# Kernel optimization log

Hardware: AMD Instinct MI355X
Metric: run time of the kernel (lower is better)

The kernel has to match this reference:

```python
import jax, jax.numpy as jnp
import numpy as np

HEADS = 16
SEQ_LEN = 2048
EMB = 1024
BATCH = 2


def setup_inputs() -> dict:
    key = jax.random.key(0)
    ks = jax.random.split(key, 5)
    s = 1.0 / np.sqrt(EMB)
    return {
        "x": jax.random.normal(ks[0], (BATCH, SEQ_LEN, EMB), dtype=jnp.float32),
        "Wk": jax.random.normal(ks[1], (EMB, EMB), dtype=jnp.float32) * s,
        "Wq": jax.random.normal(ks[2], (EMB, EMB), dtype=jnp.float32) * s,
        "Wv": jax.random.normal(ks[3], (EMB, EMB), dtype=jnp.float32) * s,
        "Wu": jax.random.normal(ks[4], (EMB, EMB), dtype=jnp.float32) * s,
        "bu": jnp.zeros((EMB,), dtype=jnp.float32),
    }


def reference(x, Wk, Wq, Wv, Wu, bu):
    B, S, E = x.shape
    H = HEADS
    D = E // H
    # projections (torch Linear: y = x @ W.T); split heads -> [B, H, S, D]
    def proj(W):
        return (x @ W.T).reshape(B, S, H, D).transpose(0, 2, 1, 3)
    q, k, v = proj(Wq), proj(Wk), proj(Wv)
    scores = jnp.einsum("bhsd,bhtd->bhst", q, k) / jnp.sqrt(jnp.float32(D))
    causal_mask = jnp.triu(jnp.ones((S, S), dtype=bool), k=1)  # True above diag
    scores = jnp.where(causal_mask, -jnp.inf, scores)
    attn = jax.nn.softmax(scores, axis=-1)
    ctx = jnp.einsum("bhst,bhtd->bhsd", attn, v)  # [B,H,S,D]
    out = ctx.transpose(0, 2, 1, 3).reshape(B, S, E)
    return out @ Wu.T + bu
```

## Files before the change

### kernel.cpp

```cpp
#include <hip/hip_runtime.h>
#include <hip/hip_bf16.h>

#define HEADS 16
#define SEQ   2048
#define EMB   1024
#define BATCH 2
#define DHEAD 64
#define MTOK  (BATCH * SEQ)

typedef __bf16 bf16x8 __attribute__((ext_vector_type(8)));
typedef float  floatx4 __attribute__((ext_vector_type(4)));

__device__ __forceinline__ void gl_lds16(const void* g, void* l) {
  __builtin_amdgcn_global_load_lds((__attribute__((address_space(1))) void*)(g),
                                   (__attribute__((address_space(3))) void*)(l), 16, 0, 0);
}

__device__ __forceinline__ unsigned short f2bf(float f) {
  __bf16 h = (__bf16)f;
  return __builtin_bit_cast(unsigned short, h);
}

__global__ __launch_bounds__(256) void cvt_kernel(
    const float* __restrict__ x,  const float* __restrict__ wq,
    const float* __restrict__ wk, const float* __restrict__ wv,
    const float* __restrict__ wu,
    unsigned short* __restrict__ xb,  unsigned short* __restrict__ wqb,
    unsigned short* __restrict__ wkb, unsigned short* __restrict__ wvb,
    unsigned short* __restrict__ wub) {
  const int g = blockIdx.x * 256 + threadIdx.x;
  const int XG = (MTOK * EMB) / 4;
  const int WG = (EMB * EMB) / 4;
  const float* src; unsigned short* dst; int off;
  if (g < XG) { src = x; dst = xb; off = g; }
  else {
    int t = g - XG; int wsel = t / WG; off = t - wsel * WG;
    const float* ss[4] = {wq, wk, wv, wu};
    unsigned short* dd[4] = {wqb, wkb, wvb, wub};
    src = ss[wsel]; dst = dd[wsel];
  }
  float4 v = ((const float4*)src)[off];
  ushort4 o;
  o.x = f2bf(v.x); o.y = f2bf(v.y); o.z = f2bf(v.z); o.w = f2bf(v.w);
  ((ushort4*)dst)[off] = o;
}

__global__ __launch_bounds__(256) void gemm_qkv(
    const unsigned short* __restrict__ xb,
    const unsigned short* __restrict__ wqb, const unsigned short* __restrict__ wkb,
    const unsigned short* __restrict__ wvb,
    unsigned short* __restrict__ Qb, unsigned short* __restrict__ Kb,
    unsigned short* __restrict__ Vt) {
  constexpr int BM = 128, BN = 64, BK = 64;
  __shared__ unsigned short As[BM * BK];
  __shared__ unsigned short Bs[3 * BN * BK];
  const int m0 = blockIdx.x * BM, n0 = blockIdx.y * BN;
  const int tid = threadIdx.x, w = tid >> 6, lane = tid & 63;
  const int quad = lane >> 4, l16 = lane & 15;
  const int wm = w >> 1, wn = w & 1;
  const int srow = lane >> 3;
  const int scol = ((lane & 7) ^ srow) * 8;
  const unsigned short* Ws[3] = {wqb, wkb, wvb};

  floatx4 acc[3][4][2] = {};

  for (int kt = 0; kt < EMB / BK; ++kt) {
    const int k0 = kt * BK;
#pragma unroll
    for (int i = 0; i < 4; ++i) {
      int r0 = i * 32 + w * 8;
      gl_lds16(xb + (size_t)(m0 + r0 + srow) * EMB + k0 + scol, &As[r0 * BK]);
    }
#pragma unroll
    for (int z = 0; z < 3; ++z)
#pragma unroll
      for (int i = 0; i < 2; ++i) {
        int r0 = i * 32 + w * 8;
        gl_lds16(Ws[z] + (size_t)(n0 + r0 + srow) * EMB + k0 + scol,
                 &Bs[z * (BN * BK) + r0 * BK]);
      }
    __syncthreads();
#pragma unroll
    for (int ks = 0; ks < 2; ++ks) {
      bf16x8 af[4];
#pragma unroll
      for (int mb = 0; mb < 4; ++mb) {
        int ra = wm * 64 + mb * 16 + l16;
        af[mb] = *(const bf16x8*)&As[ra * BK + (((ks * 4 + quad) ^ (ra & 7)) * 8)];
      }
#pragma unroll
      for (int z = 0; z < 3; ++z) {
        bf16x8 bfv[2];
#pragma unroll
        for (int nb = 0; nb < 2; ++nb) {
          int rb = wn * 32 + nb * 16 + l16;
          bfv[nb] = *(const bf16x8*)&Bs[z * (BN * BK) + rb * BK + (((ks * 4 + quad) ^ (rb & 7)) * 8)];
        }
#pragma unroll
        for (int mb = 0; mb < 4; ++mb)
#pragma unroll
          for (int nb = 0; nb < 2; ++nb)
            acc[z][mb][nb] = __builtin_amdgcn_mfma_f32_16x16x32_bf16(af[mb], bfv[nb], acc[z][mb][nb], 0, 0, 0);
      }
    }
    __syncthreads();
  }

#pragma unroll
  for (int z = 0; z < 2; ++z) {
    unsigned short* C = (z == 0) ? Qb : Kb;
    const float scale = (z == 0) ? 0.180336876f : 1.0f;
#pragma unroll
    for (int mb = 0; mb < 4; ++mb) {
#pragma unroll
      for (int nb = 0; nb < 2; ++nb) {
        int n = n0 + wn * 32 + nb * 16 + l16;
#pragma unroll
        for (int r = 0; r < 4; ++r) {
          int m = m0 + wm * 64 + mb * 16 + quad * 4 + r;
          C[(size_t)m * EMB + n] = f2bf(acc[z][mb][nb][r] * scale);
        }
      }
    }
  }
#pragma unroll
  for (int mb = 0; mb < 4; ++mb) {
    int mbase = m0 + wm * 64 + mb * 16 + quad * 4;
    int b = mbase >> 11, s = mbase & (SEQ - 1);
#pragma unroll
    for (int nb = 0; nb < 2; ++nb) {
      int n = n0 + wn * 32 + nb * 16 + l16;
      ushort4 o;
      o.x = f2bf(acc[2][mb][nb][0]); o.y = f2bf(acc[2][mb][nb][1]);
      o.z = f2bf(acc[2][mb][nb][2]); o.w = f2bf(acc[2][mb][nb][3]);
      *(ushort4*)&Vt[((size_t)b * (HEADS * DHEAD) + n) * SEQ + s] = o;
    }
  }
}

__global__ __launch_bounds__(256) void attn_kernel(
    const unsigned short* __restrict__ Qb, const unsigned short* __restrict__ Kb,
    const unsigned short* __restrict__ Vt, unsigned short* __restrict__ ctx) {
  constexpr int KT = 128;
  constexpr int PST = KT + 8;
  __shared__ unsigned short Ks[KT * DHEAD];
  __shared__ unsigned short Vs[DHEAD * KT];
  __shared__ __bf16 Ps[4 * 16 * PST];
  const int qt = 31 - blockIdx.x, bh = blockIdx.y;
  const int b = bh >> 4, h = bh & 15;
  const int q0 = qt * 64;
  const int tid = threadIdx.x, w = tid >> 6, lane = tid & 63;
  const int quad = lane >> 4, l16 = lane & 15;

  const unsigned short* Kbh = Kb + (size_t)b * SEQ * EMB + h * DHEAD;
  const unsigned short* Vbh = Vt + (size_t)bh * DHEAD * SEQ;
  __bf16* Pw = &Ps[w * (16 * PST)];

  int kq[4], kd[4], vd[4], vk[4];
#pragma unroll
  for (int i = 0; i < 4; ++i) {
    int c = i * 256 + tid;
    kq[i] = ((c >> 6) & 7) * 16 + (c & 15);
    kd[i] = ((c >> 9) << 5) + (((c >> 4) & 3) << 3);
    vd[i] = (((c >> 6) & 3) << 4) + (c & 15);
    vk[i] = (((c >> 8) & 3) << 5) + (((c >> 4) & 3) << 3);
  }

  const int myrow = q0 + w * 16 + quad * 4;
  const size_t qrow = (size_t)(b * SEQ + q0 + w * 16 + l16) * EMB + h * DHEAD;
  bf16x8 qf[2];
  qf[0] = *(const bf16x8*)&Qb[qrow + quad * 8];
  qf[1] = *(const bf16x8*)&Qb[qrow + 32 + quad * 8];

  float lsum[4] = {0.0f, 0.0f, 0.0f, 0.0f};
  floatx4 acc_o[4] = {};

  const int nkt = (qt + 2) >> 1;
  for (int ktile = 0; ktile < nkt; ++ktile) {
    const int kt0 = ktile * KT;
#pragma unroll
    for (int i = 0; i < 4; ++i) {
      gl_lds16(Kbh + (size_t)(kt0 + kq[i]) * EMB + kd[i], &Ks[(i * 256 + w * 64) * 8]);
      gl_lds16(Vbh + (size_t)vd[i] * SEQ + kt0 + vk[i], &Vs[(i * 256 + w * 64) * 8]);
    }
    __syncthreads();

    floatx4 accs[8] = {};
#pragma unroll
    for (int ks = 0; ks < 2; ++ks)
#pragma unroll
      for (int nb = 0; nb < 8; ++nb) {
        bf16x8 kf = *(const bf16x8*)&Ks[((ks * 8 + nb) * 64 + lane) * 8];
        accs[nb] = __builtin_amdgcn_mfma_f32_16x16x32_bf16(qf[ks], kf, accs[nb], 0, 0, 0);
      }

    if (ktile == nkt - 1) {
#pragma unroll
      for (int nb = 0; nb < 8; ++nb) {
        int col = kt0 + nb * 16 + l16;
#pragma unroll
        for (int r = 0; r < 4; ++r)
          if (col > myrow + r) accs[nb][r] = -1e30f;
      }
    }

#pragma unroll
    for (int r = 0; r < 4; ++r) {
#pragma unroll
      for (int nb = 0; nb < 8; ++nb) {
        float pe = exp2f(accs[nb][r]);
        Pw[(quad * 4 + r) * PST + nb * 16 + l16] = (__bf16)pe;
        lsum[r] += pe;
      }
    }

#pragma unroll
    for (int ks = 0; ks < 4; ++ks) {
      bf16x8 pf = *(const bf16x8*)&Pw[l16 * PST + ks * 32 + quad * 8];
#pragma unroll
      for (int nb = 0; nb < 4; ++nb) {
        bf16x8 vf = *(const bf16x8*)&Vs[((ks * 4 + nb) * 64 + lane) * 8];
        acc_o[nb] = __builtin_amdgcn_mfma_f32_16x16x32_bf16(pf, vf, acc_o[nb], 0, 0, 0);
      }
    }
    __syncthreads();
  }

#pragma unroll
  for (int r = 0; r < 4; ++r) {
    float rs = lsum[r];
    rs += __shfl_xor(rs, 1);
    rs += __shfl_xor(rs, 2);
    rs += __shfl_xor(rs, 4);
    rs += __shfl_xor(rs, 8);
    float inv = 1.0f / rs;
    size_t base = (size_t)(b * SEQ + myrow + r) * EMB + h * DHEAD;
#pragma unroll
    for (int nb = 0; nb < 4; ++nb)
      ctx[base + nb * 16 + l16] = f2bf(acc_o[nb][r] * inv);
  }
}

__global__ __launch_bounds__(256) void gemm_out(
    const unsigned short* __restrict__ ctx, const unsigned short* __restrict__ wub,
    const float* __restrict__ bu, float* __restrict__ out) {
  constexpr int BM = 128, BN = 64, BK = 64;
  __shared__ unsigned short As[BM * BK];
  __shared__ unsigned short Bs[BN * BK];
  const int m0 = blockIdx.x * BM, n0 = blockIdx.y * BN;
  const int tid = threadIdx.x, w = tid >> 6, lane = tid & 63;
  const int quad = lane >> 4, l16 = lane & 15;
  const int wm = w >> 1, wn = w & 1;
  const int srow = lane >> 3;
  const int scol = ((lane & 7) ^ srow) * 8;

  floatx4 acc[4][2] = {};

  for (int kt = 0; kt < EMB / BK; ++kt) {
    const int k0 = kt * BK;
#pragma unroll
    for (int i = 0; i < 4; ++i) {
      int r0 = i * 32 + w * 8;
      gl_lds16(ctx + (size_t)(m0 + r0 + srow) * EMB + k0 + scol, &As[r0 * BK]);
    }
#pragma unroll
    for (int i = 0; i < 2; ++i) {
      int r0 = i * 32 + w * 8;
      gl_lds16(wub + (size_t)(n0 + r0 + srow) * EMB + k0 + scol, &Bs[r0 * BK]);
    }
    __syncthreads();
    bf16x8 af[4][2], bfv[2][2];
#pragma unroll
    for (int mb = 0; mb < 4; ++mb) {
      int ra = wm * 64 + mb * 16 + l16;
#pragma unroll
      for (int ks = 0; ks < 2; ++ks)
        af[mb][ks] = *(const bf16x8*)&As[ra * BK + (((ks * 4 + quad) ^ (ra & 7)) * 8)];
    }
#pragma unroll
    for (int nb = 0; nb < 2; ++nb) {
      int rb = wn * 32 + nb * 16 + l16;
#pragma unroll
      for (int ks = 0; ks < 2; ++ks)
        bfv[nb][ks] = *(const bf16x8*)&Bs[rb * BK + (((ks * 4 + quad) ^ (rb & 7)) * 8)];
    }
#pragma unroll
    for (int ks = 0; ks < 2; ++ks)
#pragma unroll
      for (int mb = 0; mb < 4; ++mb)
#pragma unroll
        for (int nb = 0; nb < 2; ++nb)
          acc[mb][nb] = __builtin_amdgcn_mfma_f32_16x16x32_bf16(af[mb][ks], bfv[nb][ks], acc[mb][nb], 0, 0, 0);
    __syncthreads();
  }

#pragma unroll
  for (int mb = 0; mb < 4; ++mb) {
#pragma unroll
    for (int nb = 0; nb < 2; ++nb) {
      int n = n0 + wn * 32 + nb * 16 + l16;
      float bias = bu[n];
#pragma unroll
      for (int r = 0; r < 4; ++r) {
        int m = m0 + wm * 64 + mb * 16 + quad * 4 + r;
        out[(size_t)m * EMB + n] = acc[mb][nb][r] + bias;
      }
    }
  }
}

extern "C" void kernel_launch(void* const* d_in, const int* in_sizes, int n_in,
                              void* d_out, int out_size, void* d_ws, size_t ws_size,
                              hipStream_t stream) {
  const float* x  = (const float*)d_in[0];
  const float* Wk = (const float*)d_in[1];
  const float* Wq = (const float*)d_in[2];
  const float* Wv = (const float*)d_in[3];
  const float* Wu = (const float*)d_in[4];
  const float* bu = (const float*)d_in[5];

  char* ws = (char*)d_ws;
  const size_t MB1 = 1 << 20;
  unsigned short* xb  = (unsigned short*)(ws + 0);
  unsigned short* wqb = (unsigned short*)(ws + 8  * MB1);
  unsigned short* wkb = (unsigned short*)(ws + 10 * MB1);
  unsigned short* wvb = (unsigned short*)(ws + 12 * MB1);
  unsigned short* wub = (unsigned short*)(ws + 14 * MB1);
  unsigned short* Qb  = (unsigned short*)(ws + 16 * MB1);
  unsigned short* Kb  = (unsigned short*)(ws + 24 * MB1);
  unsigned short* Vt  = (unsigned short*)(ws + 32 * MB1);
  unsigned short* ctx = (unsigned short*)(ws + 40 * MB1);

  cvt_kernel<<<8192, 256, 0, stream>>>(x, Wq, Wk, Wv, Wu, xb, wqb, wkb, wvb, wub);
  gemm_qkv<<<dim3(32, 16), 256, 0, stream>>>(xb, wqb, wkb, wvb, Qb, Kb, Vt);
  attn_kernel<<<dim3(32, 32), 256, 0, stream>>>(Qb, Kb, Vt, ctx);
  gemm_out<<<dim3(32, 16), 256, 0, stream>>>(ctx, wub, bu, (float*)d_out);
}
```

Baseline: 231.7 us.

## Double GEMM K-tile depth and pair causal attention query tiles per block

Both GEMMs move from a K-tile of 64 to 128. The LDS swizzle widens from 8 to 16 chunks and the load mapping is reworked to match, halving the number of barrier and load rounds. The attention kernel now runs two query tiles per block (tile p and tile 31-p) so every block gets an equal causal workload, and the grid is halved. The cost is twice the LDS per GEMM block, which can lower occupancy, and only 512 attention blocks in flight.

```diff
diff --git a/kernel.cpp b/kernel.cpp
--- a/kernel.cpp
+++ b/kernel.cpp
@@ -51,15 +51,15 @@
     const unsigned short* __restrict__ wvb,
     unsigned short* __restrict__ Qb, unsigned short* __restrict__ Kb,
     unsigned short* __restrict__ Vt) {
-  constexpr int BM = 128, BN = 64, BK = 64;
+  constexpr int BM = 128, BN = 64, BK = 128;
   __shared__ unsigned short As[BM * BK];
   __shared__ unsigned short Bs[3 * BN * BK];
   const int m0 = blockIdx.x * BM, n0 = blockIdx.y * BN;
   const int tid = threadIdx.x, w = tid >> 6, lane = tid & 63;
   const int quad = lane >> 4, l16 = lane & 15;
   const int wm = w >> 1, wn = w & 1;
-  const int srow = lane >> 3;
-  const int scol = ((lane & 7) ^ srow) * 8;
+  const int srow = lane >> 4;
+  const int cphys = lane & 15;
   const unsigned short* Ws[3] = {wqb, wkb, wvb};
 
   floatx4 acc[3][4][2] = {};
@@ -67,26 +67,28 @@
   for (int kt = 0; kt < EMB / BK; ++kt) {
     const int k0 = kt * BK;
 #pragma unroll
-    for (int i = 0; i < 4; ++i) {
-      int r0 = i * 32 + w * 8;
+    for (int i = 0; i < 8; ++i) {
+      int r0 = i * 16 + w * 4;
+      int scol = (cphys ^ ((r0 + srow) & 15)) * 8;
       gl_lds16(xb + (size_t)(m0 + r0 + srow) * EMB + k0 + scol, &As[r0 * BK]);
     }
 #pragma unroll
     for (int z = 0; z < 3; ++z)
 #pragma unroll
-      for (int i = 0; i < 2; ++i) {
-        int r0 = i * 32 + w * 8;
+      for (int j = 0; j < 4; ++j) {
+        int r0 = j * 16 + w * 4;
+        int scol = (cphys ^ ((r0 + srow) & 15)) * 8;
         gl_lds16(Ws[z] + (size_t)(n0 + r0 + srow) * EMB + k0 + scol,
                  &Bs[z * (BN * BK) + r0 * BK]);
       }
     __syncthreads();
 #pragma unroll
-    for (int ks = 0; ks < 2; ++ks) {
+    for (int ks = 0; ks < 4; ++ks) {
       bf16x8 af[4];
 #pragma unroll
       for (int mb = 0; mb < 4; ++mb) {
         int ra = wm * 64 + mb * 16 + l16;
-        af[mb] = *(const bf16x8*)&As[ra * BK + (((ks * 4 + quad) ^ (ra & 7)) * 8)];
+        af[mb] = *(const bf16x8*)&As[ra * BK + (((ks * 4 + quad) ^ (ra & 15)) * 8)];
       }
 #pragma unroll
       for (int z = 0; z < 3; ++z) {
@@ -94,7 +96,7 @@
 #pragma unroll
         for (int nb = 0; nb < 2; ++nb) {
           int rb = wn * 32 + nb * 16 + l16;
-          bfv[nb] = *(const bf16x8*)&Bs[z * (BN * BK) + rb * BK + (((ks * 4 + quad) ^ (rb & 7)) * 8)];
+          bfv[nb] = *(const bf16x8*)&Bs[z * (BN * BK) + rb * BK + (((ks * 4 + quad) ^ (rb & 15)) * 8)];
         }
 #pragma unroll
         for (int mb = 0; mb < 4; ++mb)
@@ -146,9 +148,8 @@
   __shared__ unsigned short Ks[KT * DHEAD];
   __shared__ unsigned short Vs[DHEAD * KT];
   __shared__ __bf16 Ps[4 * 16 * PST];
-  const int qt = 31 - blockIdx.x, bh = blockIdx.y;
+  const int pair = blockIdx.x, bh = blockIdx.y;
   const int b = bh >> 4, h = bh & 15;
-  const int q0 = qt * 64;
   const int tid = threadIdx.x, w = tid >> 6, lane = tid & 63;
   const int quad = lane >> 4, l16 = lane & 15;
 
@@ -166,131 +167,136 @@
     vk[i] = (((c >> 8) & 3) << 5) + (((c >> 4) & 3) << 3);
   }
 
-  const int myrow = q0 + w * 16 + quad * 4;
-  const size_t qrow = (size_t)(b * SEQ + q0 + w * 16 + l16) * EMB + h * DHEAD;
-  bf16x8 qf[2];
-  qf[0] = *(const bf16x8*)&Qb[qrow + quad * 8];
-  qf[1] = *(const bf16x8*)&Qb[qrow + 32 + quad * 8];
-
-  float lsum[4] = {0.0f, 0.0f, 0.0f, 0.0f};
-  floatx4 acc_o[4] = {};
-
-  const int nkt = (qt + 2) >> 1;
-  for (int ktile = 0; ktile < nkt; ++ktile) {
-    const int kt0 = ktile * KT;
-#pragma unroll
-    for (int i = 0; i < 4; ++i) {
-      gl_lds16(Kbh + (size_t)(kt0 + kq[i]) * EMB + kd[i], &Ks[(i * 256 + w * 64) * 8]);
-      gl_lds16(Vbh + (size_t)vd[i] * SEQ + kt0 + vk[i], &Vs[(i * 256 + w * 64) * 8]);
-    }
-    __syncthreads();
-
-    floatx4 accs[8] = {};
-#pragma unroll
-    for (int ks = 0; ks < 2; ++ks)
-#pragma unroll
-      for (int nb = 0; nb < 8; ++nb) {
-        bf16x8 kf = *(const bf16x8*)&Ks[((ks * 8 + nb) * 64 + lane) * 8];
-        accs[nb] = __builtin_amdgcn_mfma_f32_16x16x32_bf16(qf[ks], kf, accs[nb], 0, 0, 0);
-      }
-
-    if (ktile == nkt - 1) {
-#pragma unroll
-      for (int nb = 0; nb < 8; ++nb) {
-        int col = kt0 + nb * 16 + l16;
-#pragma unroll
-        for (int r = 0; r < 4; ++r)
-          if (col > myrow + r) accs[nb][r] = -1e30f;
-      }
+  for (int pi = 0; pi < 2; ++pi) {
+    const int qt = pi ? (31 - pair) : pair;
+    const int q0 = qt * 64;
+    const int myrow = q0 + w * 16 + quad * 4;
+
+    const size_t qrow = (size_t)(b * SEQ + q0 + w * 16 + l16) * EMB + h * DHEAD;
+    bf16x8 qf[2];
+    qf[0] = *(const bf16x8*)&Qb[qrow + quad * 8];
+    qf[1] = *(const bf16x8*)&Qb[qrow + 32 + quad * 8];
+
+    float lsum[4] = {0.0f, 0.0f, 0.0f, 0.0f};
+    floatx4 acc_o[4] = {};
+
+    const int nkt = (qt + 2) >> 1;
+    for (int ktile = 0; ktile < nkt; ++ktile) {
+      const int kt0 = ktile * KT;
+#pragma unroll
+      for (int i = 0; i < 4; ++i) {
+        gl_lds16(Kbh + (size_t)(kt0 + kq[i]) * EMB + kd[i], &Ks[(i * 256 + w * 64) * 8]);
+        gl_lds16(Vbh + (size_t)vd[i] * SEQ + kt0 + vk[i], &Vs[(i * 256 + w * 64) * 8]);
+      }
+      __syncthreads();
+
+      floatx4 accs[8] = {};
+#pragma unroll
+      for (int ks = 0; ks < 2; ++ks)
+#pragma unroll
+        for (int nb = 0; nb < 8; ++nb) {
+          bf16x8 kf = *(const bf16x8*)&Ks[((ks * 8 + nb) * 64 + lane) * 8];
+          accs[nb] = __builtin_amdgcn_mfma_f32_16x16x32_bf16(qf[ks], kf, accs[nb], 0, 0, 0);
+        }
+
+      if (ktile == nkt - 1) {
+#pragma unroll
+        for (int nb = 0; nb < 8; ++nb) {
+          int col = kt0 + nb * 16 + l16;
+#pragma unroll
+          for (int r = 0; r < 4; ++r)
+            if (col > myrow + r) accs[nb][r] = -1e30f;
+        }
+      }
+
+#pragma unroll
+      for (int r = 0; r < 4; ++r) {
+#pragma unroll
+        for (int nb = 0; nb < 8; ++nb) {
+          float pe = exp2f(accs[nb][r]);
+          Pw[(quad * 4 + r) * PST + nb * 16 + l16] = (__bf16)pe;
+          lsum[r] += pe;
+        }
+      }
+
+#pragma unroll
+      for (int ks = 0; ks < 4; ++ks) {
+        bf16x8 pf = *(const bf16x8*)&Pw[l16 * PST + ks * 32 + quad * 8];
+#pragma unroll
+        for (int nb = 0; nb < 4; ++nb) {
+          bf16x8 vf = *(const bf16x8*)&Vs[((ks * 4 + nb) * 64 + lane) * 8];
+          acc_o[nb] = __builtin_amdgcn_mfma_f32_16x16x32_bf16(pf, vf, acc_o[nb], 0, 0, 0);
+        }
+      }
+      __syncthreads();
     }
 
 #pragma unroll
     for (int r = 0; r < 4; ++r) {
-#pragma unroll
-      for (int nb = 0; nb < 8; ++nb) {
-        float pe = exp2f(accs[nb][r]);
-        Pw[(quad * 4 + r) * PST + nb * 16 + l16] = (__bf16)pe;
-        lsum[r] += pe;
-      }
-    }
-
-#pragma unroll
-    for (int ks = 0; ks < 4; ++ks) {
-      bf16x8 pf = *(const bf16x8*)&Pw[l16 * PST + ks * 32 + quad * 8];
-#pragma unroll
-      for (int nb = 0; nb < 4; ++nb) {
-        bf16x8 vf = *(const bf16x8*)&Vs[((ks * 4 + nb) * 64 + lane) * 8];
-        acc_o[nb] = __builtin_amdgcn_mfma_f32_16x16x32_bf16(pf, vf, acc_o[nb], 0, 0, 0);
-      }
-    }
-    __syncthreads();
-  }
-
-#pragma unroll
-  for (int r = 0; r < 4; ++r) {
-    float rs = lsum[r];
-    rs += __shfl_xor(rs, 1);
-    rs += __shfl_xor(rs, 2);
-    rs += __shfl_xor(rs, 4);
-    rs += __shfl_xor(rs, 8);
-    float inv = 1.0f / rs;
-    size_t base = (size_t)(b * SEQ + myrow + r) * EMB + h * DHEAD;
-#pragma unroll
-    for (int nb = 0; nb < 4; ++nb)
-      ctx[base + nb * 16 + l16] = f2bf(acc_o[nb][r] * inv);
+      float rs = lsum[r];
+      rs += __shfl_xor(rs, 1);
+      rs += __shfl_xor(rs, 2);
+      rs += __shfl_xor(rs, 4);
+      rs += __shfl_xor(rs, 8);
+      float inv = 1.0f / rs;
+      size_t base = (size_t)(b * SEQ + myrow + r) * EMB + h * DHEAD;
+#pragma unroll
+      for (int nb = 0; nb < 4; ++nb)
+        ctx[base + nb * 16 + l16] = f2bf(acc_o[nb][r] * inv);
+    }
   }
 }
 
 __global__ __launch_bounds__(256) void gemm_out(
     const unsigned short* __restrict__ ctx, const unsigned short* __restrict__ wub,
     const float* __restrict__ bu, float* __restrict__ out) {
-  constexpr int BM = 128, BN = 64, BK = 64;
+  constexpr int BM = 128, BN = 64, BK = 128;
   __shared__ unsigned short As[BM * BK];
   __shared__ unsigned short Bs[BN * BK];
   const int m0 = blockIdx.x * BM, n0 = blockIdx.y * BN;
   const int tid = threadIdx.x, w = tid >> 6, lane = tid & 63;
   const int quad = lane >> 4, l16 = lane & 15;
   const int wm = w >> 1, wn = w & 1;
-  const int srow = lane >> 3;
-  const int scol = ((lane & 7) ^ srow) * 8;
+  const int srow = lane >> 4;
+  const int cphys = lane & 15;
 
   floatx4 acc[4][2] = {};
 
   for (int kt = 0; kt < EMB / BK; ++kt) {
     const int k0 = kt * BK;
 #pragma unroll
-    for (int i = 0; i < 4; ++i) {
-      int r0 = i * 32 + w * 8;
+    for (int i = 0; i < 8; ++i) {
+      int r0 = i * 16 + w * 4;
+      int scol = (cphys ^ ((r0 + srow) & 15)) * 8;
       gl_lds16(ctx + (size_t)(m0 + r0 + srow) * EMB + k0 + scol, &As[r0 * BK]);
     }
 #pragma unroll
-    for (int i = 0; i < 2; ++i) {
-      int r0 = i * 32 + w * 8;
+    for (int j = 0; j < 4; ++j) {
+      int r0 = j * 16 + w * 4;
+      int scol = (cphys ^ ((r0 + srow) & 15)) * 8;
       gl_lds16(wub + (size_t)(n0 + r0 + srow) * EMB + k0 + scol, &Bs[r0 * BK]);
     }
     __syncthreads();
-    bf16x8 af[4][2], bfv[2][2];
-#pragma unroll
-    for (int mb = 0; mb < 4; ++mb) {
-      int ra = wm * 64 + mb * 16 + l16;
-#pragma unroll
-      for (int ks = 0; ks < 2; ++ks)
-        af[mb][ks] = *(const bf16x8*)&As[ra * BK + (((ks * 4 + quad) ^ (ra & 7)) * 8)];
-    }
-#pragma unroll
-    for (int nb = 0; nb < 2; ++nb) {
-      int rb = wn * 32 + nb * 16 + l16;
-#pragma unroll
-      for (int ks = 0; ks < 2; ++ks)
-        bfv[nb][ks] = *(const bf16x8*)&Bs[rb * BK + (((ks * 4 + quad) ^ (rb & 7)) * 8)];
-    }
-#pragma unroll
-    for (int ks = 0; ks < 2; ++ks)
+#pragma unroll
+    for (int ks = 0; ks < 4; ++ks) {
+      bf16x8 af[4];
+#pragma unroll
+      for (int mb = 0; mb < 4; ++mb) {
+        int ra = wm * 64 + mb * 16 + l16;
+        af[mb] = *(const bf16x8*)&As[ra * BK + (((ks * 4 + quad) ^ (ra & 15)) * 8)];
+      }
+      bf16x8 bfv[2];
+#pragma unroll
+      for (int nb = 0; nb < 2; ++nb) {
+        int rb = wn * 32 + nb * 16 + l16;
+        bfv[nb] = *(const bf16x8*)&Bs[rb * BK + (((ks * 4 + quad) ^ (rb & 15)) * 8)];
+      }
 #pragma unroll
       for (int mb = 0; mb < 4; ++mb)
 #pragma unroll
         for (int nb = 0; nb < 2; ++nb)
-          acc[mb][nb] = __builtin_amdgcn_mfma_f32_16x16x32_bf16(af[mb][ks], bfv[nb][ks], acc[mb][nb], 0, 0, 0);
+          acc[mb][nb] = __builtin_amdgcn_mfma_f32_16x16x32_bf16(af[mb], bfv[nb], acc[mb][nb], 0, 0, 0);
+    }
     __syncthreads();
   }
 
@@ -333,6 +339,6 @@
 
   cvt_kernel<<<8192, 256, 0, stream>>>(x, Wq, Wk, Wv, Wu, xb, wqb, wkb, wvb, wub);
   gemm_qkv<<<dim3(32, 16), 256, 0, stream>>>(xb, wqb, wkb, wvb, Qb, Kb, Vt);
-  attn_kernel<<<dim3(32, 32), 256, 0, stream>>>(Qb, Kb, Vt, ctx);
+  attn_kernel<<<dim3(16, 32), 256, 0, stream>>>(Qb, Kb, Vt, ctx);
   gemm_out<<<dim3(32, 16), 256, 0, stream>>>(ctx, wub, bu, (float*)d_out);
 }
```

Result: faster. 200.7 us (-13.4%).
